# Performance work log

Hardware: AMD Instinct MI355X
Metric: run time of the kernel (lower is better)

Reference implementation:

```python
import jax, jax.numpy as jnp
import numpy as np

HIDDEN_DIM = 1024
NUM_EXPERTS = 8
BASE_LR = 0.5
LR_DECAY = 0.85
TOLERANCE = 0.001


def setup_inputs() -> dict:
    key = jax.random.key(0)
    ks = jax.random.split(key, 8)
    B, T, D, E = 4, 2048, HIDDEN_DIM, NUM_EXPERTS
    x_real = jax.random.normal(ks[0], (B, T, D), dtype=jnp.float32)
    x_imag = jax.random.normal(ks[1], (B, T, D), dtype=jnp.float32)
    phase_offset = jax.random.uniform(ks[2], (D,), dtype=jnp.float32) * 2.0 * np.pi
    Wg = jax.random.normal(ks[3], (D, E), dtype=jnp.float32) / np.sqrt(D)
    bg = jnp.zeros((E,), dtype=jnp.float32)
    We = jax.random.normal(ks[4], (E, D, D), dtype=jnp.float32) / np.sqrt(D)
    be = jnp.zeros((E, D), dtype=jnp.float32)
    return {"x_real": x_real, "x_imag": x_imag, "phase_offset": phase_offset,
            "Wg": Wg, "bg": bg, "We": We, "be": be, "local_iterations": 8}


def _moe(z, Wg, bg, We, be, capacity):
    # z: [N, D] complex64. Expert-choice routing on the real part.
    N, D = z.shape
    logits = z.real @ Wg + bg                     # [N, E]
    S = jax.nn.softmax(logits, axis=-1)           # [N, E]
    scores, idx = jax.lax.top_k(S.T, capacity)    # each [E, k]
    gathered = z[idx]                             # [E, k, D] complex
    out_e = jnp.einsum('ekd,edh->ekh', gathered, We.astype(z.dtype)) + be[:, None, :]
    y = jnp.zeros((N, D), z.dtype).at[idx.reshape(-1)].add(
        (scores[..., None] * out_e).reshape(-1, D))
    return y


def _build_target(z, phase_offset):
    # z: [B, T, D] complex; target[t] = z[t-1] * exp(i*phase), target[0] = z[0]
    rot = jnp.exp(1j * phase_offset)              # [D] complex64
    return jnp.concatenate([z[:, :1, :], z[:, :-1, :] * rot], axis=1)


def reference(x_real, x_imag, phase_offset, Wg, bg, We, be, local_iterations):
    B, T, D = x_real.shape
    N = B * T
    capacity = N // NUM_EXPERTS
    z0 = (x_real + 1j * x_imag).astype(jnp.complex64)  # [B, T, D]
    target = _build_target(z0, phase_offset)
    max_iters = max(1, int(local_iterations) - 1)

    def cond(carry):
        it, z, lr, done = carry
        return jnp.logical_and(it < max_iters, jnp.logical_not(done))

    def body(carry):
        it, z, lr, _ = carry
        pred = _moe(z.reshape(N, D), Wg, bg, We, be, capacity).reshape(B, T, D)
        residual = target - pred
        z = z + lr.astype(z.dtype) * residual
        res_mean = jnp.mean(jnp.abs(residual))
        return (it + 1, z, lr * LR_DECAY, res_mean < TOLERANCE)

    it0 = jnp.array(0, jnp.int32)
    lr0 = jnp.array(BASE_LR, jnp.float32)
    iters_run, z_final, _, _ = jax.lax.while_loop(cond, body, (it0, z0, lr0, jnp.array(False)))

    target_grad = _build_target(z0, phase_offset)
    pred_grad = _moe(z_final.reshape(N, D), Wg, bg, We, be, capacity).reshape(B, T, D)
    out = z_final + BASE_LR * (target_grad - pred_grad)   # [B, T, D] complex
    out_stacked = jnp.stack([out.real, out.imag], axis=-1)  # [B, T, D, 2] float32
    return out_stacked, iters_run
```

## Files before the change

kernel.cpp:

```cpp
#include <hip/hip_runtime.h>
#include <math.h>

#define ND    8388608
#define NTOK  8192
#define DIM   1024
#define NEXP  8
#define CAP   1024
#define TSEQ  2048

typedef short bf16x8 __attribute__((ext_vector_type(8)));
typedef unsigned short u16x8 __attribute__((ext_vector_type(8)));
typedef float f32x4 __attribute__((ext_vector_type(4)));

#define AS1 __attribute__((address_space(1)))
#define AS3 __attribute__((address_space(3)))

__device__ __forceinline__ void gload_lds16(const void* g, void* l) {
    __builtin_amdgcn_global_load_lds((const AS1 unsigned int*)g,
                                     (AS3 unsigned int*)l, 16, 0, 0);
}

__device__ __forceinline__ unsigned short f2bf(float x) {
    union { float f; unsigned u; } v; v.f = x;
    unsigned r = v.u + 0x7FFFu + ((v.u >> 16) & 1u);
    return (unsigned short)(r >> 16);
}
__device__ __forceinline__ float bf2f(unsigned short b) {
    union { unsigned u; float f; } v; v.u = ((unsigned)b) << 16; return v.f;
}

__global__ void k_init_small(const float* __restrict__ phase, const int* __restrict__ Lptr,
                             float* __restrict__ rc, float* __restrict__ rs,
                             int* __restrict__ ctl) {
    int d = blockIdx.x * blockDim.x + threadIdx.x;
    if (d < DIM) { rc[d] = cosf(phase[d]); rs[d] = sinf(phase[d]); }
    if (d == 0) {
        ctl[0] = 0; ctl[1] = 0;
        int L = Lptr[0]; int mi = L - 1; if (mi < 1) mi = 1;
        ctl[2] = mi;
    }
}

__global__ __launch_bounds__(256) void k_wconv(const float* __restrict__ We,
                                               unsigned short* __restrict__ Whi,
                                               unsigned short* __restrict__ Wlo) {
    __shared__ float lds[64][65];
    int e = blockIdx.z, h0 = blockIdx.x * 64, d0 = blockIdx.y * 64;
    int tid = threadIdx.x;
    #pragma unroll
    for (int q = 0; q < 16; ++q) {
        int idx = q * 256 + tid;
        int i = idx >> 6, j = idx & 63;
        lds[i][j] = We[(size_t)e * 1048576 + (size_t)(d0 + i) * 1024 + h0 + j];
    }
    __syncthreads();
    #pragma unroll
    for (int q = 0; q < 2; ++q) {
        int sid = q * 256 + tid;
        int j = sid >> 3, sp = sid & 7;
        int h = h0 + j;
        int slog = sp ^ (h & 7);
        u16x8 hi, lo;
        #pragma unroll
        for (int u = 0; u < 8; ++u) {
            float x = lds[slog * 8 + u][j];
            unsigned short hb = f2bf(x);
            hi[u] = hb;
            lo[u] = f2bf(x - bf2f(hb));
        }
        size_t o = (((size_t)(e << 10) + h) << 10) + d0 + sp * 8;
        *(u16x8*)(Whi + o) = hi;
        *(u16x8*)(Wlo + o) = lo;
    }
}

__global__ __launch_bounds__(256) void k_init_gate(
    const float* __restrict__ xr, const float* __restrict__ xi,
    unsigned short* __restrict__ zhi, unsigned short* __restrict__ zlo,
    unsigned short* __restrict__ zimB,
    const float* __restrict__ Wg, const float* __restrict__ bg,
    float* __restrict__ S, int* __restrict__ tokcnt) {
    const int w = threadIdx.x >> 6, lane = threadIdx.x & 63;
    const int n = blockIdx.x * 4 + w;
    float acc[8] = {0,0,0,0,0,0,0,0};
    #pragma unroll
    for (int q = 0; q < 4; ++q) {
        const int d0 = q * 256 + lane * 4;
        const size_t base = ((size_t)n << 10) + d0;
        float4 xv = *(const float4*)(xr + base);
        float4 iv = *(const float4*)(xi + base);
        float zz[4] = {xv.x, xv.y, xv.z, xv.w};
        float zi[4] = {iv.x, iv.y, iv.z, iv.w};
        unsigned short h4[4], l4[4], i4[4];
        #pragma unroll
        for (int j = 0; j < 4; ++j) {
            unsigned short hb = f2bf(zz[j]);
            h4[j] = hb;
            l4[j] = f2bf(zz[j] - bf2f(hb));
            i4[j] = f2bf(zi[j]);
            const float4 w0 = *(const float4*)(Wg + (d0 + j) * 8);
            const float4 w1 = *(const float4*)(Wg + (d0 + j) * 8 + 4);
            acc[0] += zz[j] * w0.x; acc[1] += zz[j] * w0.y; acc[2] += zz[j] * w0.z; acc[3] += zz[j] * w0.w;
            acc[4] += zz[j] * w1.x; acc[5] += zz[j] * w1.y; acc[6] += zz[j] * w1.z; acc[7] += zz[j] * w1.w;
        }
        *(ushort4*)(zhi + base)  = (ushort4){h4[0], h4[1], h4[2], h4[3]};
        *(ushort4*)(zlo + base)  = (ushort4){l4[0], l4[1], l4[2], l4[3]};
        *(ushort4*)(zimB + base) = (ushort4){i4[0], i4[1], i4[2], i4[3]};
    }
    #pragma unroll
    for (int off = 32; off > 0; off >>= 1)
        #pragma unroll
        for (int e = 0; e < 8; ++e) acc[e] += __shfl_xor(acc[e], off);
    if (lane == 0) {
        float m = -1e30f;
        #pragma unroll
        for (int e = 0; e < 8; ++e) { acc[e] += bg[e]; m = fmaxf(m, acc[e]); }
        float sum = 0.f;
        #pragma unroll
        for (int e = 0; e < 8; ++e) { acc[e] = expf(acc[e] - m); sum += acc[e]; }
        float inv = 1.0f / sum;
        *(float4*)(S + (n << 3))     = (float4){acc[0]*inv, acc[1]*inv, acc[2]*inv, acc[3]*inv};
        *(float4*)(S + (n << 3) + 4) = (float4){acc[4]*inv, acc[5]*inv, acc[6]*inv, acc[7]*inv};
        tokcnt[n] = 0;
    }
}

__global__ __launch_bounds__(1024) void k_route(
    const float* __restrict__ S, int* __restrict__ idxs, int* __restrict__ tokcnt,
    int* __restrict__ ent_id, const int* __restrict__ ctl, int iter) {
    if (iter >= 0 && (ctl[0] || iter >= ctl[2])) return;
    __shared__ unsigned keys[NTOK];
    __shared__ unsigned hA[2048];
    __shared__ unsigned hB[2048];
    __shared__ int sbkt, srem, sntie, scnt;
    const int e = blockIdx.x, tid = threadIdx.x;
    if (tid == 0) scnt = 0;
    for (int n = tid; n < NTOK; n += 1024) keys[n] = __float_as_uint(S[(n << 3) + e]);
    __syncthreads();

    int rem = CAP;
    unsigned pref = 0;
    #pragma unroll
    for (int lvl = 0; lvl < 3; ++lvl) {
        const int nb = (lvl == 2) ? 1024 : 2048;
        for (int i = tid; i < nb; i += 1024) hA[i] = 0;
        __syncthreads();
        for (int n = tid; n < NTOK; n += 1024) {
            unsigned k = keys[n];
            bool ok; unsigned b;
            if (lvl == 0)      { ok = true;                 b = k >> 21; }
            else if (lvl == 1) { ok = (k >> 21) == pref;    b = (k >> 10) & 2047u; }
            else               { ok = (k >> 10) == pref;    b = k & 1023u; }
            if (ok) atomicAdd(&hA[b], 1u);
        }
        __syncthreads();
        unsigned* src = hA; unsigned* dst = hB;
        for (int off = 1; off < nb; off <<= 1) {
            for (int i = tid; i < nb; i += 1024)
                dst[i] = src[i] + ((i + off < nb) ? src[i + off] : 0u);
            __syncthreads();
            unsigned* t = src; src = dst; dst = t;
        }
        for (int i = tid; i < nb; i += 1024) {
            unsigned sfi = src[i];
            unsigned sfn = (i + 1 < nb) ? src[i + 1] : 0u;
            if (sfi >= (unsigned)rem && sfn < (unsigned)rem) {
                sbkt = i; srem = rem - (int)sfn; sntie = (int)(sfi - sfn);
            }
        }
        __syncthreads();
        int b = sbkt; rem = srem;
        if (lvl == 0)      pref = (unsigned)b;
        else if (lvl == 1) pref = (pref << 11) | (unsigned)b;
        else               pref = (pref << 10) | (unsigned)b;
        __syncthreads();
    }
    const unsigned T = pref;
    const int remv = rem;
    const bool allt = (remv == sntie);

    for (int n = tid; n < NTOK; n += 1024) {
        unsigned k = keys[n];
        bool sel = (k > T);
        if (k == T) {
            if (allt) sel = true;
            else {
                int r = 0;
                int j = 0;
                for (; j + 8 <= n; j += 8) {
                    r += (int)(keys[j] == T) + (int)(keys[j+1] == T) + (int)(keys[j+2] == T)
                       + (int)(keys[j+3] == T) + (int)(keys[j+4] == T) + (int)(keys[j+5] == T)
                       + (int)(keys[j+6] == T) + (int)(keys[j+7] == T);
                }
                for (; j < n; ++j) r += (int)(keys[j] == T);
                sel = (r < remv);
            }
        }
        if (sel) {
            int slot = atomicAdd(&scnt, 1);
            int row = (e << 10) + slot;
            idxs[row] = n;
            int p = atomicAdd(&tokcnt[n], 1);
            ent_id[(n << 3) + p] = row;
        }
    }
}

__global__ __launch_bounds__(256, 2) void k_gemm_cx(
    const unsigned short* __restrict__ zhi, const unsigned short* __restrict__ zlo,
    const unsigned short* __restrict__ zimB,
    const unsigned short* __restrict__ Whi, const unsigned short* __restrict__ Wlo,
    const float* __restrict__ be, const int* __restrict__ idxs,
    float* __restrict__ outre, unsigned short* __restrict__ outim,
    const int* __restrict__ ctl, int iter) {
    if (iter >= 0 && (ctl[0] || iter >= ctl[2])) return;
    extern __shared__ unsigned short smem[];
    const int bid = blockIdx.x;
    const int e = bid & 7, bx = (bid >> 3) & 7, by = bid >> 6;
    const int tid = threadIdx.x;
    const int wid = tid >> 6, lane = tid & 63;
    const int wm = wid >> 1, wn = wid & 1;
    const int rl = lane >> 3, ch = lane & 7;
    const int swz8 = (ch ^ rl) << 3;

    int tok[16];
    if (wid < 3) {
        #pragma unroll
        for (int c = 0; c < 16; ++c)
            tok[c] = idxs[(e << 10) + by * 128 + c * 8 + rl];
    }
    const unsigned short* aplane = (wid == 0) ? zhi : (wid == 1) ? zlo : zimB;
    unsigned short* albase = smem + (wid << 13);

    const int wrowbase = (e << 10) + bx * 128;
    const unsigned short* whsrc = Whi + (((size_t)(wrowbase + rl)) << 10) + (ch << 3);
    const unsigned short* wlsrc = Wlo + (((size_t)(wrowbase + rl)) << 10) + (ch << 3);

    f32x4 accre[4][4], accim[4][4];
    #pragma unroll
    for (int a = 0; a < 4; ++a)
        #pragma unroll
        for (int b = 0; b < 4; ++b) {
            accre[a][b] = (f32x4){0.f, 0.f, 0.f, 0.f};
            accim[a][b] = (f32x4){0.f, 0.f, 0.f, 0.f};
        }

    for (int kt = 0; kt < DIM; kt += 64) {
        if (kt) __syncthreads();
        if (wid < 3) {
            #pragma unroll
            for (int c = 0; c < 16; ++c)
                gload_lds16(aplane + (((size_t)tok[c]) << 10) + kt + swz8, albase + c * 512);
        } else {
            #pragma unroll
            for (int c = 0; c < 16; ++c)
                gload_lds16(whsrc + kt + ((size_t)c << 13), smem + 24576 + c * 512);
        }
        #pragma unroll
        for (int q = 0; q < 4; ++q) {
            int c = (wid << 2) + q;
            gload_lds16(wlsrc + kt + ((size_t)c << 13), smem + 32768 + c * 512);
        }
        __syncthreads();
        #pragma unroll
        for (int ks = 0; ks < 2; ++ks) {
            const int slog = (ks << 2) + (lane >> 4);
            const int swz = (slog ^ (lane & 7)) << 3;
            bf16x8 ah[4], al[4], am[4], bh[4], bl[4];
            #pragma unroll
            for (int mi = 0; mi < 4; ++mi) {
                int off = ((wm * 64 + mi * 16 + (lane & 15)) << 6) + swz;
                ah[mi] = *(const bf16x8*)&smem[off];
                al[mi] = *(const bf16x8*)&smem[8192 + off];
                am[mi] = *(const bf16x8*)&smem[16384 + off];
            }
            #pragma unroll
            for (int ni = 0; ni < 4; ++ni) {
                int off = ((wn * 64 + ni * 16 + (lane & 15)) << 6) + swz;
                bh[ni] = *(const bf16x8*)&smem[24576 + off];
                bl[ni] = *(const bf16x8*)&smem[32768 + off];
            }
            #pragma unroll
            for (int mi = 0; mi < 4; ++mi)
                #pragma unroll
                for (int ni = 0; ni < 4; ++ni) {
                    accre[mi][ni] = __builtin_amdgcn_mfma_f32_16x16x32_bf16(ah[mi], bh[ni], accre[mi][ni], 0, 0, 0);
                    accre[mi][ni] = __builtin_amdgcn_mfma_f32_16x16x32_bf16(ah[mi], bl[ni], accre[mi][ni], 0, 0, 0);
                    accre[mi][ni] = __builtin_amdgcn_mfma_f32_16x16x32_bf16(al[mi], bh[ni], accre[mi][ni], 0, 0, 0);
                    accim[mi][ni] = __builtin_amdgcn_mfma_f32_16x16x32_bf16(am[mi], bh[ni], accim[mi][ni], 0, 0, 0);
                }
        }
    }
    const int colbase = bx * 128 + wn * 64 + (lane & 15);
    float bev[4];
    #pragma unroll
    for (int ni = 0; ni < 4; ++ni) bev[ni] = be[(e << 10) + colbase + ni * 16];
    const int rowloc = by * 128 + wm * 64 + ((lane >> 4) << 2);
    float* obr = outre + (((size_t)(e << 10) + rowloc) << 10) + colbase;
    unsigned short* obi = outim + (((size_t)(e << 10) + rowloc) << 10) + colbase;
    #pragma unroll
    for (int mi = 0; mi < 4; ++mi)
        #pragma unroll
        for (int rg = 0; rg < 4; ++rg) {
            size_t ro = (size_t)(mi * 16 + rg) << 10;
            #pragma unroll
            for (int ni = 0; ni < 4; ++ni) {
                obr[ro + ni * 16] = accre[mi][ni][rg] + bev[ni];
                obi[ro + ni * 16] = f2bf(accim[mi][ni][rg]);
            }
        }
}

__global__ __launch_bounds__(256) void k_resid_gate(
    unsigned short* __restrict__ zhi, unsigned short* __restrict__ zlo,
    unsigned short* __restrict__ zimB,
    const float* __restrict__ xr, const float* __restrict__ xi,
    const float* __restrict__ rc, const float* __restrict__ rs,
    const float* __restrict__ outre, const unsigned short* __restrict__ outim,
    int* __restrict__ tokcnt, const int* __restrict__ ent_id,
    float* __restrict__ S, const float* __restrict__ Wg, const float* __restrict__ bg,
    float lr, float* __restrict__ partial, const int* __restrict__ ctl, int iter) {
    if (ctl[0] || iter >= ctl[2]) return;
    __shared__ float wred[4][8];
    const int n = blockIdx.x;
    const int tid = threadIdx.x;
    const int d0 = tid << 2;
    const int kc = tokcnt[n];
    const int4 e0 = *(const int4*)(ent_id + (n << 3));
    const int4 e1 = *(const int4*)(ent_id + (n << 3) + 4);
    const int rows[8] = {e0.x, e0.y, e0.z, e0.w, e1.x, e1.y, e1.z, e1.w};

    float pr[4] = {0,0,0,0}, pm[4] = {0,0,0,0};
    #pragma unroll
    for (int k = 0; k < 8; ++k) {
        if (k < kc) {
            const int row = rows[k];
            const float s = S[(n << 3) + (row >> 10)];
            const float4 vr = *(const float4*)(outre + ((size_t)row << 10) + d0);
            const ushort4 vi = *(const ushort4*)(outim + ((size_t)row << 10) + d0);
            pr[0] += s * vr.x; pr[1] += s * vr.y; pr[2] += s * vr.z; pr[3] += s * vr.w;
            pm[0] += s * bf2f(vi.x); pm[1] += s * bf2f(vi.y); pm[2] += s * bf2f(vi.z); pm[3] += s * bf2f(vi.w);
        }
    }
    const size_t base = ((size_t)n << 10) + d0;
    const int t = n & (TSEQ - 1);
    float tr[4], ti[4];
    if (t == 0) {
        float4 a = *(const float4*)(xr + base), b = *(const float4*)(xi + base);
        tr[0]=a.x; tr[1]=a.y; tr[2]=a.z; tr[3]=a.w;
        ti[0]=b.x; ti[1]=b.y; ti[2]=b.z; ti[3]=b.w;
    } else {
        float4 a = *(const float4*)(xr + base - DIM), b = *(const float4*)(xi + base - DIM);
        float4 c = *(const float4*)(rc + d0), s4 = *(const float4*)(rs + d0);
        tr[0]=a.x*c.x-b.x*s4.x; tr[1]=a.y*c.y-b.y*s4.y; tr[2]=a.z*c.z-b.z*s4.z; tr[3]=a.w*c.w-b.w*s4.w;
        ti[0]=a.x*s4.x+b.x*c.x; ti[1]=a.y*s4.y+b.y*c.y; ti[2]=a.z*s4.z+b.z*c.z; ti[3]=a.w*s4.w+b.w*c.w;
    }
    ushort4 h4 = *(const ushort4*)(zhi + base);
    ushort4 l4 = *(const ushort4*)(zlo + base);
    ushort4 zi4 = *(const ushort4*)(zimB + base);
    float zrv[4] = {bf2f(h4.x)+bf2f(l4.x), bf2f(h4.y)+bf2f(l4.y),
                    bf2f(h4.z)+bf2f(l4.z), bf2f(h4.w)+bf2f(l4.w)};
    unsigned short ziv[4] = {zi4.x, zi4.y, zi4.z, zi4.w};
    unsigned short hn[4], ln[4], zo[4];
    float lsum = 0.f;
    float lac[8] = {0,0,0,0,0,0,0,0};
    #pragma unroll
    for (int j = 0; j < 4; ++j) {
        float rr = tr[j] - pr[j];
        float ri = ti[j] - pm[j];
        float zn = zrv[j] + lr * rr;
        unsigned short hb = f2bf(zn);
        hn[j] = hb;
        ln[j] = f2bf(zn - bf2f(hb));
        zo[j] = f2bf(bf2f(ziv[j]) + lr * ri);
        lsum += sqrtf(rr * rr + ri * ri);
        const float4 w0 = *(const float4*)(Wg + (d0 + j) * 8);
        const float4 w1 = *(const float4*)(Wg + (d0 + j) * 8 + 4);
        lac[0] += zn * w0.x; lac[1] += zn * w0.y; lac[2] += zn * w0.z; lac[3] += zn * w0.w;
        lac[4] += zn * w1.x; lac[5] += zn * w1.y; lac[6] += zn * w1.z; lac[7] += zn * w1.w;
    }
    *(ushort4*)(zhi + base)  = (ushort4){hn[0], hn[1], hn[2], hn[3]};
    *(ushort4*)(zlo + base)  = (ushort4){ln[0], ln[1], ln[2], ln[3]};
    *(ushort4*)(zimB + base) = (ushort4){zo[0], zo[1], zo[2], zo[3]};

    const int w = tid >> 6, lane = tid & 63;
    #pragma unroll
    for (int off = 32; off > 0; off >>= 1) {
        lsum += __shfl_xor(lsum, off);
        #pragma unroll
        for (int e = 0; e < 8; ++e) lac[e] += __shfl_xor(lac[e], off);
    }
    if (lane == 0) {
        #pragma unroll
        for (int e = 0; e < 8; ++e) wred[w][e] = lac[e];
        partial[(n << 2) + w] = lsum;
    }
    __syncthreads();
    if (tid == 0) {
        float lg[8];
        float m = -1e30f;
        #pragma unroll
        for (int e = 0; e < 8; ++e) {
            lg[e] = wred[0][e] + wred[1][e] + wred[2][e] + wred[3][e] + bg[e];
            m = fmaxf(m, lg[e]);
        }
        float sum = 0.f;
        #pragma unroll
        for (int e = 0; e < 8; ++e) { lg[e] = expf(lg[e] - m); sum += lg[e]; }
        float inv = 1.0f / sum;
        *(float4*)(S + (n << 3))     = (float4){lg[0]*inv, lg[1]*inv, lg[2]*inv, lg[3]*inv};
        *(float4*)(S + (n << 3) + 4) = (float4){lg[4]*inv, lg[5]*inv, lg[6]*inv, lg[7]*inv};
        tokcnt[n] = 0;
    }
}

__global__ __launch_bounds__(1024) void k_finalize(
    const float* __restrict__ partial, int* __restrict__ ctl, int iter) {
    if (ctl[0] || iter >= ctl[2]) return;
    __shared__ float red[16];
    float s = 0.f;
    for (int i = threadIdx.x; i < NTOK * 4; i += 1024) s += partial[i];
    #pragma unroll
    for (int off = 32; off > 0; off >>= 1) s += __shfl_xor(s, off);
    if ((threadIdx.x & 63) == 0) red[threadIdx.x >> 6] = s;
    __syncthreads();
    if (threadIdx.x == 0) {
        float tot = 0.f;
        #pragma unroll
        for (int w = 0; w < 16; ++w) tot += red[w];
        ctl[1] = iter + 1;
        if (tot * (1.0f / (float)ND) < 0.001f) ctl[0] = 1;
    }
}

__global__ __launch_bounds__(256) void k_final_zupd(
    unsigned short* __restrict__ zhi, unsigned short* __restrict__ zlo,
    unsigned short* __restrict__ zimB,
    const float* __restrict__ xr, const float* __restrict__ xi,
    const float* __restrict__ rc, const float* __restrict__ rs,
    const float* __restrict__ outre, const unsigned short* __restrict__ outim,
    const int* __restrict__ tokcnt, const int* __restrict__ ent_id,
    const float* __restrict__ S) {
    const int n = blockIdx.x;
    const int tid = threadIdx.x;
    const int d0 = tid << 2;
    const int kc = tokcnt[n];
    const int4 e0 = *(const int4*)(ent_id + (n << 3));
    const int4 e1 = *(const int4*)(ent_id + (n << 3) + 4);
    const int rows[8] = {e0.x, e0.y, e0.z, e0.w, e1.x, e1.y, e1.z, e1.w};
    float pr[4] = {0,0,0,0}, pm[4] = {0,0,0,0};
    #pragma unroll
    for (int k = 0; k < 8; ++k) {
        if (k < kc) {
            const int row = rows[k];
            const float s = S[(n << 3) + (row >> 10)];
            const float4 vr = *(const float4*)(outre + ((size_t)row << 10) + d0);
            const ushort4 vi = *(const ushort4*)(outim + ((size_t)row << 10) + d0);
            pr[0] += s * vr.x; pr[1] += s * vr.y; pr[2] += s * vr.z; pr[3] += s * vr.w;
            pm[0] += s * bf2f(vi.x); pm[1] += s * bf2f(vi.y); pm[2] += s * bf2f(vi.z); pm[3] += s * bf2f(vi.w);
        }
    }
    const size_t base = ((size_t)n << 10) + d0;
    const int t = n & (TSEQ - 1);
    float tr[4], ti[4];
    if (t == 0) {
        float4 a = *(const float4*)(xr + base), b = *(const float4*)(xi + base);
        tr[0]=a.x; tr[1]=a.y; tr[2]=a.z; tr[3]=a.w;
        ti[0]=b.x; ti[1]=b.y; ti[2]=b.z; ti[3]=b.w;
    } else {
        float4 a = *(const float4*)(xr + base - DIM), b = *(const float4*)(xi + base - DIM);
        float4 c = *(const float4*)(rc + d0), s4 = *(const float4*)(rs + d0);
        tr[0]=a.x*c.x-b.x*s4.x; tr[1]=a.y*c.y-b.y*s4.y; tr[2]=a.z*c.z-b.z*s4.z; tr[3]=a.w*c.w-b.w*s4.w;
        ti[0]=a.x*s4.x+b.x*c.x; ti[1]=a.y*s4.y+b.y*c.y; ti[2]=a.z*s4.z+b.z*c.z; ti[3]=a.w*s4.w+b.w*c.w;
    }
    ushort4 h4 = *(const ushort4*)(zhi + base);
    ushort4 l4 = *(const ushort4*)(zlo + base);
    ushort4 zi4 = *(const ushort4*)(zimB + base);
    float zrv[4] = {bf2f(h4.x)+bf2f(l4.x), bf2f(h4.y)+bf2f(l4.y),
                    bf2f(h4.z)+bf2f(l4.z), bf2f(h4.w)+bf2f(l4.w)};
    unsigned short ziv[4] = {zi4.x, zi4.y, zi4.z, zi4.w};
    unsigned short hn[4], ln[4], zo[4];
    #pragma unroll
    for (int j = 0; j < 4; ++j) {
        float zn = zrv[j] + 0.5f * (tr[j] - pr[j]);
        unsigned short hb = f2bf(zn);
        hn[j] = hb;
        ln[j] = f2bf(zn - bf2f(hb));
        zo[j] = f2bf(bf2f(ziv[j]) + 0.5f * (ti[j] - pm[j]));
    }
    *(ushort4*)(zhi + base)  = (ushort4){hn[0], hn[1], hn[2], hn[3]};
    *(ushort4*)(zlo + base)  = (ushort4){ln[0], ln[1], ln[2], ln[3]};
    *(ushort4*)(zimB + base) = (ushort4){zo[0], zo[1], zo[2], zo[3]};
}

__global__ void k_write_out(const unsigned short* __restrict__ zhi,
                            const unsigned short* __restrict__ zlo,
                            const unsigned short* __restrict__ zimB,
                            float* __restrict__ out, const int* __restrict__ ctl) {
    int i = blockIdx.x * blockDim.x + threadIdx.x;
    if (i >= ND) return;
    out[2 * i]     = bf2f(zhi[i]) + bf2f(zlo[i]);
    out[2 * i + 1] = bf2f(zimB[i]);
    if (i == 0) out[(size_t)2 * ND] = (float)ctl[1];
}

extern "C" void kernel_launch(void* const* d_in, const int* in_sizes, int n_in,
                              void* d_out, int out_size, void* d_ws, size_t ws_size,
                              hipStream_t stream) {
    (void)in_sizes; (void)n_in; (void)out_size; (void)ws_size;
    const float* x_real = (const float*)d_in[0];
    const float* x_imag = (const float*)d_in[1];
    const float* phase  = (const float*)d_in[2];
    const float* Wg     = (const float*)d_in[3];
    const float* bg     = (const float*)d_in[4];
    const float* We     = (const float*)d_in[5];
    const float* be     = (const float*)d_in[6];
    const int*   Lptr   = (const int*)d_in[7];

    char* wsb = (char*)d_ws;
    unsigned short* zhi  = (unsigned short*)wsb;
    unsigned short* zlo  = (unsigned short*)(wsb + 16777216);
    unsigned short* zimB = (unsigned short*)(wsb + 33554432);
    unsigned short* Whi  = (unsigned short*)(wsb + 50331648);
    unsigned short* Wlo  = (unsigned short*)(wsb + 67108864);
    float*    S       = (float*)(wsb + 83886080);
    int*      ent_id  = (int*)  (wsb + 84148224);
    int*      idxs    = (int*)  (wsb + 84410368);
    int*      tokcnt  = (int*)  (wsb + 84443136);
    float*    partial = (float*)(wsb + 84475904);
    float*    rc      = (float*)(wsb + 84606976);
    float*    rs      = (float*)(wsb + 84611072);
    int*      ctl     = (int*)  (wsb + 84615168);

    float*          outre = (float*)d_out;
    unsigned short* outim = (unsigned short*)((char*)d_out + 33554432);

    k_init_small<<<4, 256, 0, stream>>>(phase, Lptr, rc, rs, ctl);
    k_wconv<<<dim3(16, 16, 8), 256, 0, stream>>>(We, Whi, Wlo);
    k_init_gate<<<NTOK / 4, 256, 0, stream>>>(x_real, x_imag, zhi, zlo, zimB, Wg, bg, S, tokcnt);

    const size_t gemm_lds = 40960 * sizeof(unsigned short);
    float lr = 0.5f;
    for (int it = 0; it < 7; ++it) {
        k_route<<<NEXP, 1024, 0, stream>>>(S, idxs, tokcnt, ent_id, ctl, it);
        k_gemm_cx<<<512, 256, gemm_lds, stream>>>(zhi, zlo, zimB, Whi, Wlo, be, idxs,
                                                  outre, outim, ctl, it);
        k_resid_gate<<<NTOK, 256, 0, stream>>>(zhi, zlo, zimB, x_real, x_imag, rc, rs,
                                               outre, outim, tokcnt, ent_id, S, Wg, bg,
                                               lr, partial, ctl, it);
        k_finalize<<<1, 1024, 0, stream>>>(partial, ctl, it);
        lr *= 0.85f;
    }

    k_route<<<NEXP, 1024, 0, stream>>>(S, idxs, tokcnt, ent_id, ctl, -1);
    k_gemm_cx<<<512, 256, gemm_lds, stream>>>(zhi, zlo, zimB, Whi, Wlo, be, idxs,
                                              outre, outim, ctl, -1);
    k_final_zupd<<<NTOK, 256, 0, stream>>>(zhi, zlo, zimB, x_real, x_imag, rc, rs,
                                           outre, outim, tokcnt, ent_id, S);
    k_write_out<<<ND / 256, 256, 0, stream>>>(zhi, zlo, zimB, (float*)d_out, ctl);
}
```

Baseline: 1.132 ms.

## Load zimB and Wlo operands directly from global to shrink LDS footprint

The kernel stops staging the imaginary-activation plane and the low-half weight plane in LDS. Those MFMA operands are now read straight from global memory inside the inner k-loop, using precomputed token and weight row indices. The global-to-LDS copies for the remaining three planes are spread evenly over all four waves. This cuts shared memory from 80 KB to 48 KB, and launch bounds are raised to three blocks per CU to gain occupancy. The cost is global-memory latency on the MFMA critical path with no LDS reuse for those operands, plus a tighter register budget that could cause spills.

Result: slower. 3.442 ms (+204.1%).

```diff
diff --git a/kernel.cpp b/kernel.cpp
--- a/kernel.cpp
+++ b/kernel.cpp
@@ -206,7 +206,7 @@
     }
 }
 
-__global__ __launch_bounds__(256, 2) void k_gemm_cx(
+__global__ __launch_bounds__(256, 3) void k_gemm_cx(
     const unsigned short* __restrict__ zhi, const unsigned short* __restrict__ zlo,
     const unsigned short* __restrict__ zimB,
     const unsigned short* __restrict__ Whi, const unsigned short* __restrict__ Wlo,
@@ -223,18 +223,29 @@
     const int rl = lane >> 3, ch = lane & 7;
     const int swz8 = (ch ^ rl) << 3;
 
-    int tok[16];
-    if (wid < 3) {
-        #pragma unroll
-        for (int c = 0; c < 16; ++c)
-            tok[c] = idxs[(e << 10) + by * 128 + c * 8 + rl];
-    }
-    const unsigned short* aplane = (wid == 0) ? zhi : (wid == 1) ? zlo : zimB;
-    unsigned short* albase = smem + (wid << 13);
-
-    const int wrowbase = (e << 10) + bx * 128;
-    const unsigned short* whsrc = Whi + (((size_t)(wrowbase + rl)) << 10) + (ch << 3);
-    const unsigned short* wlsrc = Wlo + (((size_t)(wrowbase + rl)) << 10) + (ch << 3);
+    const unsigned short* sp[12];
+    int dofs[12];
+    #pragma unroll
+    for (int i = 0; i < 12; ++i) {
+        int idx = wid * 12 + i;
+        int T = idx >> 4, c = idx & 15;
+        int row;
+        const unsigned short* plane;
+        int col;
+        if (T == 0)      { plane = zhi; row = idxs[(e << 10) + by * 128 + c * 8 + rl]; col = swz8; }
+        else if (T == 1) { plane = zlo; row = idxs[(e << 10) + by * 128 + c * 8 + rl]; col = swz8; }
+        else             { plane = Whi; row = (e << 10) + bx * 128 + c * 8 + rl;       col = ch << 3; }
+        sp[i] = plane + ((size_t)row << 10) + col;
+        dofs[i] = (T << 13) + c * 512;
+    }
+
+    int tokam[4], wrow[4];
+    #pragma unroll
+    for (int mi = 0; mi < 4; ++mi)
+        tokam[mi] = idxs[(e << 10) + by * 128 + wm * 64 + mi * 16 + (lane & 15)];
+    #pragma unroll
+    for (int ni = 0; ni < 4; ++ni)
+        wrow[ni] = (e << 10) + bx * 128 + wn * 64 + ni * 16 + (lane & 15);
 
     f32x4 accre[4][4], accim[4][4];
     #pragma unroll
@@ -247,20 +258,9 @@
 
     for (int kt = 0; kt < DIM; kt += 64) {
         if (kt) __syncthreads();
-        if (wid < 3) {
-            #pragma unroll
-            for (int c = 0; c < 16; ++c)
-                gload_lds16(aplane + (((size_t)tok[c]) << 10) + kt + swz8, albase + c * 512);
-        } else {
-            #pragma unroll
-            for (int c = 0; c < 16; ++c)
-                gload_lds16(whsrc + kt + ((size_t)c << 13), smem + 24576 + c * 512);
-        }
-        #pragma unroll
-        for (int q = 0; q < 4; ++q) {
-            int c = (wid << 2) + q;
-            gload_lds16(wlsrc + kt + ((size_t)c << 13), smem + 32768 + c * 512);
-        }
+        #pragma unroll
+        for (int i = 0; i < 12; ++i)
+            gload_lds16(sp[i] + kt, smem + dofs[i]);
         __syncthreads();
         #pragma unroll
         for (int ks = 0; ks < 2; ++ks) {
@@ -272,13 +272,13 @@
                 int off = ((wm * 64 + mi * 16 + (lane & 15)) << 6) + swz;
                 ah[mi] = *(const bf16x8*)&smem[off];
                 al[mi] = *(const bf16x8*)&smem[8192 + off];
-                am[mi] = *(const bf16x8*)&smem[16384 + off];
+                am[mi] = *(const bf16x8*)(zimB + (((size_t)tokam[mi]) << 10) + kt + (slog << 3));
             }
             #pragma unroll
             for (int ni = 0; ni < 4; ++ni) {
                 int off = ((wn * 64 + ni * 16 + (lane & 15)) << 6) + swz;
-                bh[ni] = *(const bf16x8*)&smem[24576 + off];
-                bl[ni] = *(const bf16x8*)&smem[32768 + off];
+                bh[ni] = *(const bf16x8*)&smem[16384 + off];
+                bl[ni] = *(const bf16x8*)(Wlo + (((size_t)wrow[ni]) << 10) + kt + swz);
             }
             #pragma unroll
             for (int mi = 0; mi < 4; ++mi)
@@ -539,7 +539,7 @@
     k_wconv<<<dim3(16, 16, 8), 256, 0, stream>>>(We, Whi, Wlo);
     k_init_gate<<<NTOK / 4, 256, 0, stream>>>(x_real, x_imag, zhi, zlo, zimB, Wg, bg, S, tokcnt);
 
-    const size_t gemm_lds = 40960 * sizeof(unsigned short);
+    const size_t gemm_lds = 24576 * sizeof(unsigned short);
     float lr = 0.5f;
     for (int it = 0; it < 7; ++it) {
         k_route<<<NEXP, 1024, 0, stream>>>(S, idxs, tokcnt, ent_id, ctl, it);
```
